# Kernel optimization log

Measured on AMD Instinct MI355X. Metric: run time of the kernel, lower is better.

The kernel has to match this reference:

```python
import jax, jax.numpy as jnp
import numpy as np

N = 50000
E = 800000
IN_C, HID, HEADS, CLS = 128, 64, 5, 40
NEG_SLOPE = 0.2


def gat_conv(h, src, dst, W, a_src, a_dst, bias, heads, out_c, concat):
    n = h.shape[0]
    hp = (h @ W).reshape(n, heads, out_c)            # [N,H,C]
    a_s = jnp.sum(hp * a_src, axis=-1)               # [N,H]
    a_d = jnp.sum(hp * a_dst, axis=-1)               # [N,H]
    e = jax.nn.leaky_relu(a_s[src] + a_d[dst], NEG_SLOPE)  # [Etot,H]
    m = jax.ops.segment_max(e, dst, num_segments=n)  # segment softmax over dst
    e = jnp.exp(e - m[dst])
    s = jax.ops.segment_sum(e, dst, num_segments=n)
    alpha = e / (s[dst] + 1e-16)                     # [Etot,H]
    msg = hp[src] * alpha[:, :, None]                # [Etot,H,C]
    out = jax.ops.segment_sum(msg, dst, num_segments=n)
    if concat:
        out = out.reshape(n, heads * out_c)
    else:
        out = out.mean(axis=1)
    return out + bias


def setup_inputs() -> dict:
    key = jax.random.key(0)
    ks = jax.random.split(key, 12)
    x = jax.random.normal(ks[0], (N, IN_C), dtype=jnp.float32)
    edge_index = jax.random.randint(ks[1], (2, E), 0, N, dtype=jnp.int64)
    g = 0.1
    return {
        "x": x,
        "edge_index": edge_index,
        "emb_W": jax.random.normal(ks[2], (IN_C, HID), jnp.float32) * g,
        "emb_b": jnp.zeros((HID,), jnp.float32),
        "W1": jax.random.normal(ks[3], (HID, HEADS * HID), jnp.float32) * g,
        "att_src1": jax.random.normal(ks[4], (HEADS, HID), jnp.float32) * g,
        "att_dst1": jax.random.normal(ks[5], (HEADS, HID), jnp.float32) * g,
        "b1": jnp.zeros((HEADS * HID,), jnp.float32),
        "W2": jax.random.normal(ks[6], (HEADS * HID, HEADS * CLS), jnp.float32) * g,
        "att_src2": jax.random.normal(ks[7], (HEADS, CLS), jnp.float32) * g,
        "att_dst2": jax.random.normal(ks[8], (HEADS, CLS), jnp.float32) * g,
        "b2": jnp.zeros((CLS,), jnp.float32),
    }


def reference(x, edge_index, emb_W, emb_b, W1, att_src1, att_dst1, b1,
              W2, att_src2, att_dst2, b2):
    n = x.shape[0]
    loops = jnp.arange(n, dtype=edge_index.dtype)
    src = jnp.concatenate([edge_index[0], loops])  # PyG adds self-loops
    dst = jnp.concatenate([edge_index[1], loops])
    h = x @ emb_W + emb_b
    emb = h
    # dropout skipped (eval mode)
    h = jax.nn.elu(gat_conv(h, src, dst, W1, att_src1, att_dst1, b1, HEADS, HID, True))
    h = gat_conv(h, src, dst, W2, att_src2, att_dst2, b2, HEADS, CLS, False)
    return emb, jax.nn.log_softmax(h, axis=1)
```

## Files before the change

kernel.cpp:

```cpp
#include <hip/hip_runtime.h>
#include <math.h>

constexpr int N_NODES = 50000;
constexpr int E_EDGES = 800000;
constexpr int ETOT    = E_EDGES + N_NODES;
constexpr int IN_C    = 128;
constexpr int HID     = 64;
constexpr int HEADS   = 5;
constexpr int CLS     = 40;
constexpr int SLOTW   = 96;
constexpr float NEG_SLOPE = 0.2f;

typedef __attribute__((ext_vector_type(8))) short short8;
typedef __attribute__((ext_vector_type(4))) float float4v;
typedef __attribute__((ext_vector_type(2))) float f32x2;

__device__ __forceinline__ float lrelu(float v) {
    return v > 0.f ? v : NEG_SLOPE * v;
}
__device__ __forceinline__ float bf2f(unsigned short u) {
    return __uint_as_float(((unsigned)u) << 16);
}
__device__ __forceinline__ f32x2 bfp2f(unsigned u) {
    f32x2 r;
    r.x = __uint_as_float(u << 16);
    r.y = __uint_as_float(u & 0xFFFF0000u);
    return r;
}
__device__ __forceinline__ unsigned short f2bf(float f) {
    unsigned u = __float_as_uint(f);
    return (unsigned short)((u + 0x7fffu + ((u >> 16) & 1u)) >> 16);
}

__device__ __forceinline__ void pack_one(const float* __restrict__ B,
                                         unsigned short* __restrict__ Bp,
                                         int N, int KS, int t)
{
    int lane = t & 63;
    int f = (t >> 6) & 3;
    int rest = t >> 8;
    int ks = rest % KS;
    int nt = rest / KS;
    int n = nt * 64 + f * 16 + (lane & 15);
    int kbase = ks * 32 + (lane >> 4) * 8;
    unsigned short vals[8];
    #pragma unroll
    for (int j = 0; j < 8; j++) {
        float v = (n < N) ? B[(long)(kbase + j) * N + n] : 0.f;
        vals[j] = f2bf(v);
    }
    *(ushort4*)(Bp + (long)t * 8)     = make_ushort4(vals[0], vals[1], vals[2], vals[3]);
    *(ushort4*)(Bp + (long)t * 8 + 4) = make_ushort4(vals[4], vals[5], vals[6], vals[7]);
}

__global__ void build_graph(const int* __restrict__ ei, int* __restrict__ cnt,
                            unsigned short* __restrict__ slots,
                            const float* __restrict__ W0, const float* __restrict__ W1,
                            const float* __restrict__ W2,
                            const float* __restrict__ att1s, const float* __restrict__ att1d,
                            const float* __restrict__ att2s, const float* __restrict__ att2d,
                            unsigned short* __restrict__ Bp0,
                            unsigned short* __restrict__ Bp1,
                            unsigned short* __restrict__ Bp2,
                            float* __restrict__ u1s, float* __restrict__ u1d,
                            float* __restrict__ u2s, float* __restrict__ u2d)
{
    int t = blockIdx.x * blockDim.x + threadIdx.x;
    if (t < 13824) {
        if (t < 1024)      pack_one(W0, Bp0, 64,  4,  t);
        else if (t < 3584) pack_one(W1, Bp1, 320, 2,  t - 1024);
        else               pack_one(W2, Bp2, 200, 10, t - 3584);
    } else if (t < 14464) {
        int i = t - 13824;
        bool isd = i >= 320;
        int j = isd ? i - 320 : i;
        int h = j >> 6, k = j & 63;
        const float* att = isd ? att1d : att1s;
        float sum = 0.f;
        for (int c = 0; c < 64; c++)
            sum += W1[k * 320 + h * 64 + c] * att[h * 64 + c];
        (isd ? u1d : u1s)[j] = sum;
    } else if (t < 17664) {
        int i = t - 14464;
        bool isd = i >= 1600;
        int j = isd ? i - 1600 : i;
        int h = j / 320, k = j % 320;
        const float* att = isd ? att2d : att2s;
        float sum = 0.f;
        for (int c = 0; c < 40; c++)
            sum += W2[k * 200 + h * 40 + c] * att[h * 40 + c];
        (isd ? u2d : u2s)[j] = sum;
    }
    if (t >= ETOT) return;
    int s, d;
    if (t < E_EDGES) { s = ei[t]; d = ei[E_EDGES + t]; }
    else             { s = d = t - E_EDGES; }
    int pos = atomicAdd(&cnt[d], 1);
    if (pos < SLOTW) slots[d * SLOTW + pos] = (unsigned short)s;
}

__global__ __launch_bounds__(256) void gemm_mfma_emb(
    const float* __restrict__ A, const unsigned short* __restrict__ Bp,
    const float* __restrict__ bias,
    const float* __restrict__ u1s, const float* __restrict__ u1d,
    float* __restrict__ Cf, unsigned short* __restrict__ Cb,
    float* __restrict__ asd, int M)
{
    const int K = 128, KS = 4;
    const int w = threadIdx.x >> 6, lane = threadIdx.x & 63;
    const int cl = lane & 15, kq = lane >> 4;
    int rowA = blockIdx.x * 64 + w * 16 + cl;
    if (rowA >= M) rowA = M - 1;
    const float* ap = A + (long)rowA * K + kq * 8;
    const unsigned short* bp = Bp + lane * 8;
    float4v acc[4] = {};
    #pragma unroll
    for (int ks = 0; ks < KS; ks++) {
        float4 u0 = *(const float4*)(ap + ks * 32);
        float4 u1 = *(const float4*)(ap + ks * 32 + 4);
        short8 a;
        a[0] = f2bf(u0.x); a[1] = f2bf(u0.y); a[2] = f2bf(u0.z); a[3] = f2bf(u0.w);
        a[4] = f2bf(u1.x); a[5] = f2bf(u1.y); a[6] = f2bf(u1.z); a[7] = f2bf(u1.w);
        #pragma unroll
        for (int f = 0; f < 4; f++) {
            short8 b = *(const short8*)(bp + ks * 2048 + f * 512);
            acc[f] = __builtin_amdgcn_mfma_f32_16x16x32_bf16(a, b, acc[f], 0, 0, 0);
        }
    }
    int rbase = blockIdx.x * 64 + w * 16 + kq * 4;
    float bc4[4];
    #pragma unroll
    for (int f = 0; f < 4; f++) {
        int col = f * 16 + cl;
        float bc = bias[col];
        bc4[f] = bc;
        #pragma unroll
        for (int r = 0; r < 4; r++) {
            int row = rbase + r;
            if (row < M) {
                float v = acc[f][r] + bc;
                Cf[(long)row * 64 + col] = v;
                Cb[(long)row * 64 + col] = f2bf(v);
            }
        }
    }
    #pragma unroll
    for (int h = 0; h < HEADS; h++) {
        float us[4], ud[4];
        #pragma unroll
        for (int f = 0; f < 4; f++) {
            us[f] = u1s[h * 64 + f * 16 + cl];
            ud[f] = u1d[h * 64 + f * 16 + cl];
        }
        #pragma unroll
        for (int r = 0; r < 4; r++) {
            float ps = 0.f, pd = 0.f;
            #pragma unroll
            for (int f = 0; f < 4; f++) {
                float v = acc[f][r] + bc4[f];
                ps += v * us[f];
                pd += v * ud[f];
            }
            #pragma unroll
            for (int off = 1; off < 16; off <<= 1) {
                ps += __shfl_xor(ps, off);
                pd += __shfl_xor(pd, off);
            }
            int row = rbase + r;
            if (cl == 0 && row < M) {
                asd[row * 16 + h]     = ps;
                asd[row * 16 + 8 + h] = pd;
            }
        }
    }
}

__global__ __launch_bounds__(256) void aggr1_new(
    const int* __restrict__ cnt, const unsigned short* __restrict__ slots,
    const float* __restrict__ asd,
    const unsigned short* __restrict__ emb, unsigned short* __restrict__ e_out)
{
    __shared__ float alph[4][64 * 8];
    int wid = (blockIdx.x * blockDim.x + threadIdx.x) >> 6;
    int w = threadIdx.x >> 6;
    int lane = threadIdx.x & 63;
    if (wid >= N_NODES) return;
    int deg = cnt[wid];
    if (deg > SLOTW) deg = SLOTW;
    const unsigned short* myslot = slots + wid * SLOTW;

    float adh[HEADS];
    #pragma unroll
    for (int h = 0; h < HEADS; h++) adh[h] = asd[wid * 16 + 8 + h];

    const char* embB = (const char*)emb;

    if (deg <= 64) {
        bool has = lane < deg;
        int s = has ? (int)myslot[lane] : 0;
        int rowoff = s * 128;
        float4 s4 = *(const float4*)(asd + s * 16);
        float  s5 = asd[s * 16 + 4];
        float v[HEADS], mx[HEADS], sm[HEADS];
        v[0] = has ? lrelu(s4.x + adh[0]) : -1e30f;
        v[1] = has ? lrelu(s4.y + adh[1]) : -1e30f;
        v[2] = has ? lrelu(s4.z + adh[2]) : -1e30f;
        v[3] = has ? lrelu(s4.w + adh[3]) : -1e30f;
        v[4] = has ? lrelu(s5   + adh[4]) : -1e30f;
        #pragma unroll
        for (int h = 0; h < HEADS; h++) mx[h] = v[h];
        if (deg <= 32) {
            #pragma unroll
            for (int h = 0; h < HEADS; h++)
                #pragma unroll
                for (int off = 16; off; off >>= 1)
                    mx[h] = fmaxf(mx[h], __shfl_xor(mx[h], off));
        } else {
            #pragma unroll
            for (int h = 0; h < HEADS; h++)
                #pragma unroll
                for (int off = 32; off; off >>= 1)
                    mx[h] = fmaxf(mx[h], __shfl_xor(mx[h], off));
        }
        #pragma unroll
        for (int h = 0; h < HEADS; h++) {
            float e = has ? __expf(v[h] - mx[h]) : 0.f;
            v[h] = e;
            sm[h] = e;
        }
        if (deg <= 32) {
            #pragma unroll
            for (int h = 0; h < HEADS; h++)
                #pragma unroll
                for (int off = 16; off; off >>= 1)
                    sm[h] += __shfl_xor(sm[h], off);
        } else {
            #pragma unroll
            for (int h = 0; h < HEADS; h++)
                #pragma unroll
                for (int off = 32; off; off >>= 1)
                    sm[h] += __shfl_xor(sm[h], off);
        }
        #pragma unroll
        for (int h = 0; h < HEADS; h++)
            alph[w][lane * 8 + h] = v[h] / (sm[h] + 1e-16f);

        const int g = lane >> 4, cl16 = lane & 15;
        f32x2 av[HEADS][2] = {};
        int nE8 = (deg + 7) & ~7;
        for (int i = 0; i < nE8; i += 8) {
            int e0 = i + g, e1 = i + 4 + g;
            int off0 = __shfl(rowoff, e0);
            int off1 = __shfl(rowoff, e1);
            uint2 q0 = *(const uint2*)(embB + off0 + cl16 * 8);
            uint2 q1 = *(const uint2*)(embB + off1 + cl16 * 8);
            float4 b0 = *(const float4*)&alph[w][e0 * 8];
            float  b4 = alph[w][e0 * 8 + 4];
            float4 c0 = *(const float4*)&alph[w][e1 * 8];
            float  c4 = alph[w][e1 * 8 + 4];
            f32x2 f0a = bfp2f(q0.x), f0b = bfp2f(q0.y);
            f32x2 f1a = bfp2f(q1.x), f1b = bfp2f(q1.y);
            av[0][0] += f0a * b0.x; av[0][1] += f0b * b0.x;
            av[1][0] += f0a * b0.y; av[1][1] += f0b * b0.y;
            av[2][0] += f0a * b0.z; av[2][1] += f0b * b0.z;
            av[3][0] += f0a * b0.w; av[3][1] += f0b * b0.w;
            av[4][0] += f0a * b4;   av[4][1] += f0b * b4;
            av[0][0] += f1a * c0.x; av[0][1] += f1b * c0.x;
            av[1][0] += f1a * c0.y; av[1][1] += f1b * c0.y;
            av[2][0] += f1a * c0.z; av[2][1] += f1b * c0.z;
            av[3][0] += f1a * c0.w; av[3][1] += f1b * c0.w;
            av[4][0] += f1a * c4;   av[4][1] += f1b * c4;
        }
        #pragma unroll
        for (int h = 0; h < HEADS; h++)
            #pragma unroll
            for (int p = 0; p < 2; p++) {
                float tx = av[h][p].x, ty = av[h][p].y;
                tx += __shfl_xor(tx, 16); tx += __shfl_xor(tx, 32);
                ty += __shfl_xor(ty, 16); ty += __shfl_xor(ty, 32);
                av[h][p].x = tx; av[h][p].y = ty;
            }
        if (g == 0) {
            #pragma unroll
            for (int h = 0; h < HEADS; h++) {
                ushort4 o = make_ushort4(f2bf(av[h][0].x), f2bf(av[h][0].y),
                                         f2bf(av[h][1].x), f2bf(av[h][1].y));
                *(ushort4*)(e_out + (long)wid * 320 + h * 64 + cl16 * 4) = o;
            }
        }
    } else {
        float acc[HEADS] = {};
        float mx[HEADS], inv[HEADS], sm[HEADS] = {};
        #pragma unroll
        for (int h = 0; h < HEADS; h++) mx[h] = -1e30f;
        for (int e = lane; e < deg; e += 64) {
            int s = myslot[e];
            #pragma unroll
            for (int h = 0; h < HEADS; h++)
                mx[h] = fmaxf(mx[h], lrelu(asd[s * 16 + h] + adh[h]));
        }
        #pragma unroll
        for (int h = 0; h < HEADS; h++)
            #pragma unroll
            for (int off = 32; off; off >>= 1)
                mx[h] = fmaxf(mx[h], __shfl_xor(mx[h], off));
        for (int e = lane; e < deg; e += 64) {
            int s = myslot[e];
            #pragma unroll
            for (int h = 0; h < HEADS; h++)
                sm[h] += __expf(lrelu(asd[s * 16 + h] + adh[h]) - mx[h]);
        }
        #pragma unroll
        for (int h = 0; h < HEADS; h++) {
            #pragma unroll
            for (int off = 32; off; off >>= 1)
                sm[h] += __shfl_xor(sm[h], off);
            inv[h] = 1.f / (sm[h] + 1e-16f);
        }
        for (int e = 0; e < deg; e++) {
            int s0 = myslot[e];
            float fv = bf2f(*(const unsigned short*)(embB + s0 * 128 + lane * 2));
            #pragma unroll
            for (int h = 0; h < HEADS; h++) {
                float a0 = __expf(lrelu(asd[s0 * 16 + h] + adh[h]) - mx[h]) * inv[h];
                acc[h] += fv * a0;
            }
        }
        #pragma unroll
        for (int h = 0; h < HEADS; h++)
            e_out[(long)wid * 320 + h * 64 + lane] = f2bf(acc[h]);
    }
}

__global__ __launch_bounds__(256) void gemm_mix_l2(
    const unsigned short* __restrict__ A, const unsigned short* __restrict__ Bp1,
    const unsigned short* __restrict__ Bp2, const float* __restrict__ bias,
    const float* __restrict__ u2s, const float* __restrict__ u2d,
    unsigned short* __restrict__ hp2, float* __restrict__ asd, int M)
{
    constexpr int LDP = 328;
    __shared__ unsigned short tile[64 * LDP];
    const int w = threadIdx.x >> 6, lane = threadIdx.x & 63;
    const int cl = lane & 15, kq = lane >> 4;
    int rowA = blockIdx.x * 64 + w * 16 + cl;
    if (rowA >= M) rowA = M - 1;
    const unsigned short* ap = A + (long)rowA * 320;
    const unsigned short* bp1 = Bp1 + lane * 8;

    float4v acc[20] = {};
    #pragma unroll
    for (int nt = 0; nt < 5; nt++)
        #pragma unroll
        for (int ks = 0; ks < 2; ks++) {
            short8 a = *(const short8*)(ap + nt * 64 + ks * 32 + kq * 8);
            #pragma unroll
            for (int f = 0; f < 4; f++) {
                short8 b = *(const short8*)(bp1 + (nt * 2 + ks) * 2048 + f * 512);
                acc[nt * 4 + f] =
                    __builtin_amdgcn_mfma_f32_16x16x32_bf16(a, b, acc[nt * 4 + f], 0, 0, 0);
            }
        }
    int rbase = blockIdx.x * 64 + w * 16 + kq * 4;
    const int lrow = w * 16 + kq * 4;
    #pragma unroll
    for (int nt = 0; nt < 5; nt++)
        #pragma unroll
        for (int f = 0; f < 4; f++) {
            int col = nt * 64 + f * 16 + cl;
            float bc = bias[col];
            #pragma unroll
            for (int r = 0; r < 4; r++) {
                float v = acc[nt * 4 + f][r] + bc;
                v = v > 0.f ? v : __expf(v) - 1.f;
                acc[nt * 4 + f][r] = v;
                tile[(lrow + r) * LDP + col] = f2bf(v);
            }
        }
    #pragma unroll
    for (int h = 0; h < HEADS; h++) {
        float us[20], ud[20];
        #pragma unroll
        for (int nt = 0; nt < 5; nt++)
            #pragma unroll
            for (int f = 0; f < 4; f++) {
                us[nt * 4 + f] = u2s[h * 320 + nt * 64 + f * 16 + cl];
                ud[nt * 4 + f] = u2d[h * 320 + nt * 64 + f * 16 + cl];
            }
        #pragma unroll
        for (int r = 0; r < 4; r++) {
            float ps = 0.f, pd = 0.f;
            #pragma unroll
            for (int j = 0; j < 20; j++) {
                ps += acc[j][r] * us[j];
                pd += acc[j][r] * ud[j];
            }
            #pragma unroll
            for (int off = 1; off < 16; off <<= 1) {
                ps += __shfl_xor(ps, off);
                pd += __shfl_xor(pd, off);
            }
            int row = rbase + r;
            if (cl == 0 && row < M) {
                asd[row * 16 + h]     = ps;
                asd[row * 16 + 8 + h] = pd;
            }
        }
    }

    const unsigned short* bp2 = Bp2 + lane * 8;
    const unsigned short* arow = tile + (w * 16 + cl) * LDP;
    float4v acc2[16] = {};
    #pragma unroll
    for (int ks = 0; ks < 10; ks++) {
        short8 a2 = *(const short8*)(arow + ks * 32 + kq * 8);
        #pragma unroll
        for (int nt = 0; nt < 4; nt++)
            #pragma unroll
            for (int f = 0; f < 4; f++) {
                short8 b = *(const short8*)(bp2 + (nt * 10 + ks) * 2048 + f * 512);
                acc2[nt * 4 + f] =
                    __builtin_amdgcn_mfma_f32_16x16x32_bf16(a2, b, acc2[nt * 4 + f], 0, 0, 0);
            }
    }
    #pragma unroll
    for (int nt = 0; nt < 4; nt++)
        #pragma unroll
        for (int f = 0; f < 4; f++) {
            int col = nt * 64 + f * 16 + cl;
            if (col >= 200) continue;
            #pragma unroll
            for (int r = 0; r < 4; r++) {
                int row = rbase + r;
                if (row < M) hp2[(long)row * 200 + col] = f2bf(acc2[nt * 4 + f][r]);
            }
        }
}

__global__ __launch_bounds__(256) void aggr2_fused(
    const int* __restrict__ cnt, const unsigned short* __restrict__ slots,
    const float* __restrict__ asd,
    const unsigned short* __restrict__ hp, const float* __restrict__ bias,
    float* __restrict__ out)
{
    __shared__ float alph[4][320];
    int wid = (blockIdx.x * blockDim.x + threadIdx.x) >> 6;
    int w = threadIdx.x >> 6;
    int lane = threadIdx.x & 63;
    if (wid >= N_NODES) return;
    int deg = cnt[wid];
    if (deg > SLOTW) deg = SLOTW;
    const unsigned short* myslot = slots + wid * SLOTW;

    float adh[HEADS];
    #pragma unroll
    for (int h = 0; h < HEADS; h++) adh[h] = asd[wid * 16 + 8 + h];

    const bool act = lane < 50;
    const int ch4 = lane * 4;
    const int hq  = act ? lane / 10 : 0;
    const char* hpB = (const char*)hp;
    f32x2 acc01 = {0.f, 0.f}, acc23 = {0.f, 0.f};

    if (deg <= 64) {
        bool has = lane < deg;
        int s = has ? (int)myslot[lane] : 0;
        int rowoff = s * 400;
        float4 s4 = *(const float4*)(asd + s * 16);
        float  s5 = asd[s * 16 + 4];
        float v[HEADS], mx[HEADS], sm[HEADS];
        v[0] = has ? lrelu(s4.x + adh[0]) : -1e30f;
        v[1] = has ? lrelu(s4.y + adh[1]) : -1e30f;
        v[2] = has ? lrelu(s4.z + adh[2]) : -1e30f;
        v[3] = has ? lrelu(s4.w + adh[3]) : -1e30f;
        v[4] = has ? lrelu(s5   + adh[4]) : -1e30f;
        #pragma unroll
        for (int h = 0; h < HEADS; h++) mx[h] = v[h];
        if (deg <= 32) {
            #pragma unroll
            for (int h = 0; h < HEADS; h++)
                #pragma unroll
                for (int off = 16; off; off >>= 1)
                    mx[h] = fmaxf(mx[h], __shfl_xor(mx[h], off));
        } else {
            #pragma unroll
            for (int h = 0; h < HEADS; h++)
                #pragma unroll
                for (int off = 32; off; off >>= 1)
                    mx[h] = fmaxf(mx[h], __shfl_xor(mx[h], off));
        }
        #pragma unroll
        for (int h = 0; h < HEADS; h++) {
            float e = has ? __expf(v[h] - mx[h]) : 0.f;
            v[h] = e;
            sm[h] = e;
        }
        if (deg <= 32) {
            #pragma unroll
            for (int h = 0; h < HEADS; h++)
                #pragma unroll
                for (int off = 16; off; off >>= 1)
                    sm[h] += __shfl_xor(sm[h], off);
        } else {
            #pragma unroll
            for (int h = 0; h < HEADS; h++)
                #pragma unroll
                for (int off = 32; off; off >>= 1)
                    sm[h] += __shfl_xor(sm[h], off);
        }
        if (has) {
            #pragma unroll
            for (int h = 0; h < HEADS; h++)
                alph[w][lane * 5 + h] = 0.2f * v[h] / (sm[h] + 1e-16f);
        }
        int i = 0;
        for (; i + 7 < deg; i += 8) {
            uint2 q[8]; float a[8];
            #pragma unroll
            for (int k = 0; k < 8; k++) {
                int off = __shfl(rowoff, i + k);
                q[k] = act ? *(const uint2*)(hpB + off + ch4 * 2)
                           : make_uint2(0u, 0u);
                a[k] = alph[w][(i + k) * 5 + hq];
            }
            #pragma unroll
            for (int k = 0; k < 8; k++) {
                f32x2 fa = bfp2f(q[k].x), fb = bfp2f(q[k].y);
                acc01 += fa * a[k];
                acc23 += fb * a[k];
            }
        }
        for (; i < deg; i++) {
            int off = __shfl(rowoff, i);
            if (act) {
                uint2 q0 = *(const uint2*)(hpB + off + ch4 * 2);
                float a0 = alph[w][i * 5 + hq];
                f32x2 fa = bfp2f(q0.x), fb = bfp2f(q0.y);
                acc01 += fa * a0;
                acc23 += fb * a0;
            }
        }
    } else {
        float mx[HEADS], inv[HEADS], sm[HEADS] = {};
        #pragma unroll
        for (int h = 0; h < HEADS; h++) mx[h] = -1e30f;
        for (int e = lane; e < deg; e += 64) {
            int s = myslot[e];
            #pragma unroll
            for (int h = 0; h < HEADS; h++)
                mx[h] = fmaxf(mx[h], lrelu(asd[s * 16 + h] + adh[h]));
        }
        #pragma unroll
        for (int h = 0; h < HEADS; h++)
            #pragma unroll
            for (int off = 32; off; off >>= 1)
                mx[h] = fmaxf(mx[h], __shfl_xor(mx[h], off));
        for (int e = lane; e < deg; e += 64) {
            int s = myslot[e];
            #pragma unroll
            for (int h = 0; h < HEADS; h++)
                sm[h] += __expf(lrelu(asd[s * 16 + h] + adh[h]) - mx[h]);
        }
        #pragma unroll
        for (int h = 0; h < HEADS; h++) {
            #pragma unroll
            for (int off = 32; off; off >>= 1)
                sm[h] += __shfl_xor(sm[h], off);
            inv[h] = 0.2f / (sm[h] + 1e-16f);
        }
        for (int e = 0; e < deg; e++) {
            int s0 = myslot[e];
            if (act) {
                uint2 q0 = *(const uint2*)(hpB + s0 * 400 + ch4 * 2);
                float a0 = __expf(lrelu(asd[s0 * 16 + hq] + adh[hq]) - mx[hq]) * inv[hq];
                f32x2 fa = bfp2f(q0.x), fb = bfp2f(q0.y);
                acc01 += fa * a0;
                acc23 += fb * a0;
            }
        }
    }

    float acc0 = acc01.x, acc1 = acc01.y, acc2 = acc23.x, acc3 = acc23.y;
    float r0 = acc0, r1 = acc1, r2 = acc2, r3 = acc3;
    #pragma unroll
    for (int h5 = 1; h5 < 5; h5++) {
        int sl = (lane + 10 * h5) & 63;
        r0 += __shfl(acc0, sl);
        r1 += __shfl(acc1, sl);
        r2 += __shfl(acc2, sl);
        r3 += __shfl(acc3, sl);
    }

    float vb0 = -1e30f, vb1 = -1e30f, vb2 = -1e30f, vb3 = -1e30f;
    if (lane < 10) {
        vb0 = r0 + bias[ch4 + 0];
        vb1 = r1 + bias[ch4 + 1];
        vb2 = r2 + bias[ch4 + 2];
        vb3 = r3 + bias[ch4 + 3];
    }
    float mxv = fmaxf(fmaxf(vb0, vb1), fmaxf(vb2, vb3));
    #pragma unroll
    for (int off = 32; off; off >>= 1)
        mxv = fmaxf(mxv, __shfl_xor(mxv, off));
    float sme = 0.f;
    if (lane < 10)
        sme = __expf(vb0 - mxv) + __expf(vb1 - mxv) +
              __expf(vb2 - mxv) + __expf(vb3 - mxv);
    #pragma unroll
    for (int off = 32; off; off >>= 1)
        sme += __shfl_xor(sme, off);
    float ls = mxv + __logf(sme);
    if (lane < 10) {
        float4 o = make_float4(vb0 - ls, vb1 - ls, vb2 - ls, vb3 - ls);
        *(float4*)(out + (long)wid * CLS + ch4) = o;
    }
}

extern "C" void kernel_launch(void* const* d_in, const int* in_sizes, int n_in,
                              void* d_out, int out_size, void* d_ws, size_t ws_size,
                              hipStream_t stream)
{
    const float* x     = (const float*)d_in[0];
    const int*   ei    = (const int*)d_in[1];
    const float* emb_W = (const float*)d_in[2];
    const float* emb_b = (const float*)d_in[3];
    const float* W1    = (const float*)d_in[4];
    const float* as1   = (const float*)d_in[5];
    const float* ad1   = (const float*)d_in[6];
    const float* b1    = (const float*)d_in[7];
    const float* W2    = (const float*)d_in[8];
    const float* as2   = (const float*)d_in[9];
    const float* ad2   = (const float*)d_in[10];
    const float* b2    = (const float*)d_in[11];

    float* out_emb = (float*)d_out;
    float* out_cls = (float*)d_out + (size_t)N_NODES * HID;

    char* ws = (char*)d_ws;
    unsigned short* e_agg  = (unsigned short*)(ws);
    unsigned short* hp2b   = (unsigned short*)(ws + 32000000);
    float*          asd1   = (float*)(ws + 52000000);
    float*          asd2   = (float*)(ws + 55200000);
    unsigned short* embb   = (unsigned short*)(ws + 64000000);
    unsigned short* Bp0    = (unsigned short*)(ws + 74400000);
    unsigned short* Bp1    = (unsigned short*)(ws + 74500000);
    unsigned short* Bp2    = (unsigned short*)(ws + 74600000);
    float*          u1s    = (float*)(ws + 74800000);
    float*          u1d    = (float*)(ws + 74810000);
    float*          u2s    = (float*)(ws + 74820000);
    float*          u2d    = (float*)(ws + 74830000);
    int*            cnt    = (int*)(ws + 74840000);
    unsigned short* slots  = (unsigned short*)(ws + 75100000);

    const dim3 blk(256);
    const int eb  = (ETOT + 255) / 256;
    const int nb4 = (N_NODES + 3) / 4;
    const int mgrid = (N_NODES + 63) / 64;

    hipMemsetAsync(cnt, 0, (size_t)N_NODES * 4, stream);
    build_graph<<<eb, blk, 0, stream>>>(ei, cnt, slots, emb_W, W1, W2,
                                        as1, ad1, as2, ad2,
                                        Bp0, Bp1, Bp2, u1s, u1d, u2s, u2d);

    gemm_mfma_emb<<<mgrid, blk, 0, stream>>>(x, Bp0, emb_b, u1s, u1d,
                                             out_emb, embb, asd1, N_NODES);

    aggr1_new<<<nb4, blk, 0, stream>>>(cnt, slots, asd1, embb, e_agg);

    gemm_mix_l2<<<mgrid, blk, 0, stream>>>(e_agg, Bp1, Bp2, b1, u2s, u2d,
                                           hp2b, asd2, N_NODES);

    aggr2_fused<<<nb4, blk, 0, stream>>>(cnt, slots, asd2, hp2b, b2, out_cls);
}
```

Baseline: 364.7 us.

## Split layer-2 GEMM across wave pairs and compute attention logits via MFMA

Restructures the fused layer-1 transform + layer-2 GEMM kernel so each block handles 32 rows, with two waves per 16-row band splitting the N dimension of both GEMMs and sharing the ELU output through LDS with a block barrier. The per-head attention projections (previously scalar dot products plus shuffles over 20 accumulators) are folded into an extra packed bf16 B matrix, so they come out of one additional MFMA column tile. This cuts per-wave register pressure (launch bounds raised to 5 waves) and scalar work. In exchange it adds a __syncthreads and computes the attention logits in bf16 precision rather than fp32.

```diff
diff --git a/kernel.cpp b/kernel.cpp
--- a/kernel.cpp
+++ b/kernel.cpp
@@ -63,7 +63,7 @@
                             unsigned short* __restrict__ Bp1,
                             unsigned short* __restrict__ Bp2,
                             float* __restrict__ u1s, float* __restrict__ u1d,
-                            float* __restrict__ u2s, float* __restrict__ u2d)
+                            unsigned short* __restrict__ Bs)
 {
     int t = blockIdx.x * blockDim.x + threadIdx.x;
     if (t < 13824) {
@@ -80,16 +80,27 @@
         for (int c = 0; c < 64; c++)
             sum += W1[k * 320 + h * 64 + c] * att[h * 64 + c];
         (isd ? u1d : u1s)[j] = sum;
-    } else if (t < 17664) {
+    } else if (t < 15104) {
         int i = t - 14464;
-        bool isd = i >= 1600;
-        int j = isd ? i - 1600 : i;
-        int h = j / 320, k = j % 320;
-        const float* att = isd ? att2d : att2s;
-        float sum = 0.f;
-        for (int c = 0; c < 40; c++)
-            sum += W2[k * 200 + h * 40 + c] * att[h * 40 + c];
-        (isd ? u2d : u2s)[j] = sum;
+        int lane = i & 63, ks = i >> 6;
+        int n = lane & 15, kq = lane >> 4;
+        unsigned short vals[8];
+        #pragma unroll
+        for (int j = 0; j < 8; j++) {
+            int k = ks * 32 + kq * 8 + j;
+            float sum = 0.f;
+            if (n < 5) {
+                for (int c = 0; c < 40; c++)
+                    sum += W2[k * 200 + n * 40 + c] * att2s[n * 40 + c];
+            } else if (n >= 8 && n < 13) {
+                int h = n - 8;
+                for (int c = 0; c < 40; c++)
+                    sum += W2[k * 200 + h * 40 + c] * att2d[h * 40 + c];
+            }
+            vals[j] = f2bf(sum);
+        }
+        *(ushort4*)(Bs + (long)i * 8)     = make_ushort4(vals[0], vals[1], vals[2], vals[3]);
+        *(ushort4*)(Bs + (long)i * 8 + 4) = make_ushort4(vals[4], vals[5], vals[6], vals[7]);
     }
     if (t >= ETOT) return;
     int s, d;
@@ -332,106 +343,120 @@
     }
 }
 
-__global__ __launch_bounds__(256) void gemm_mix_l2(
+__global__ __launch_bounds__(256, 5) void gemm_mix_l2(
     const unsigned short* __restrict__ A, const unsigned short* __restrict__ Bp1,
     const unsigned short* __restrict__ Bp2, const float* __restrict__ bias,
-    const float* __restrict__ u2s, const float* __restrict__ u2d,
+    const unsigned short* __restrict__ Bs,
     unsigned short* __restrict__ hp2, float* __restrict__ asd, int M)
 {
     constexpr int LDP = 328;
-    __shared__ unsigned short tile[64 * LDP];
-    const int w = threadIdx.x >> 6, lane = threadIdx.x & 63;
+    __shared__ unsigned short tile[32 * LDP];
+    const int wid = threadIdx.x >> 6, lane = threadIdx.x & 63;
+    const int band = wid >> 1, half = wid & 1;
     const int cl = lane & 15, kq = lane >> 4;
-    int rowA = blockIdx.x * 64 + w * 16 + cl;
+    int rowA = blockIdx.x * 32 + band * 16 + cl;
     if (rowA >= M) rowA = M - 1;
     const unsigned short* ap = A + (long)rowA * 320;
     const unsigned short* bp1 = Bp1 + lane * 8;
 
-    float4v acc[20] = {};
-    #pragma unroll
-    for (int nt = 0; nt < 5; nt++)
-        #pragma unroll
-        for (int ks = 0; ks < 2; ks++) {
-            short8 a = *(const short8*)(ap + nt * 64 + ks * 32 + kq * 8);
+    const int rbase = blockIdx.x * 32 + band * 16 + kq * 4;
+    const int lrow = band * 16 + kq * 4;
+
+    if (half == 0) {
+        float4v acc[12] = {};
+        #pragma unroll
+        for (int i = 0; i < 3; i++)
+            #pragma unroll
+            for (int ks = 0; ks < 2; ks++) {
+                short8 a = *(const short8*)(ap + i * 64 + ks * 32 + kq * 8);
+                #pragma unroll
+                for (int f = 0; f < 4; f++) {
+                    short8 b = *(const short8*)(bp1 + (i * 2 + ks) * 2048 + f * 512);
+                    acc[i * 4 + f] =
+                        __builtin_amdgcn_mfma_f32_16x16x32_bf16(a, b, acc[i * 4 + f], 0, 0, 0);
+                }
+            }
+        #pragma unroll
+        for (int i = 0; i < 3; i++)
             #pragma unroll
             for (int f = 0; f < 4; f++) {
-                short8 b = *(const short8*)(bp1 + (nt * 2 + ks) * 2048 + f * 512);
-                acc[nt * 4 + f] =
-                    __builtin_amdgcn_mfma_f32_16x16x32_bf16(a, b, acc[nt * 4 + f], 0, 0, 0);
-            }
-        }
-    int rbase = blockIdx.x * 64 + w * 16 + kq * 4;
-    const int lrow = w * 16 + kq * 4;
-    #pragma unroll
-    for (int nt = 0; nt < 5; nt++)
-        #pragma unroll
-        for (int f = 0; f < 4; f++) {
-            int col = nt * 64 + f * 16 + cl;
-            float bc = bias[col];
-            #pragma unroll
-            for (int r = 0; r < 4; r++) {
-                float v = acc[nt * 4 + f][r] + bc;
-                v = v > 0.f ? v : __expf(v) - 1.f;
-                acc[nt * 4 + f][r] = v;
-                tile[(lrow + r) * LDP + col] = f2bf(v);
-            }
-        }
-    #pragma unroll
-    for (int h = 0; h < HEADS; h++) {
-        float us[20], ud[20];
-        #pragma unroll
-        for (int nt = 0; nt < 5; nt++)
+                int col = i * 64 + f * 16 + cl;
+                float bc = bias[col];
+                #pragma unroll
+                for (int r = 0; r < 4; r++) {
+                    float v = acc[i * 4 + f][r] + bc;
+                    v = v > 0.f ? v : __expf(v) - 1.f;
+                    tile[(lrow + r) * LDP + col] = f2bf(v);
+                }
+            }
+    } else {
+        float4v acc[8] = {};
+        #pragma unroll
+        for (int i = 0; i < 2; i++)
+            #pragma unroll
+            for (int ks = 0; ks < 2; ks++) {
+                short8 a = *(const short8*)(ap + (3 + i) * 64 + ks * 32 + kq * 8);
+                #pragma unroll
+                for (int f = 0; f < 4; f++) {
+                    short8 b = *(const short8*)(bp1 + ((3 + i) * 2 + ks) * 2048 + f * 512);
+                    acc[i * 4 + f] =
+                        __builtin_amdgcn_mfma_f32_16x16x32_bf16(a, b, acc[i * 4 + f], 0, 0, 0);
+                }
+            }
+        #pragma unroll
+        for (int i = 0; i < 2; i++)
             #pragma unroll
             for (int f = 0; f < 4; f++) {
-                us[nt * 4 + f] = u2s[h * 320 + nt * 64 + f * 16 + cl];
-                ud[nt * 4 + f] = u2d[h * 320 + nt * 64 + f * 16 + cl];
-            }
-        #pragma unroll
-        for (int r = 0; r < 4; r++) {
-            float ps = 0.f, pd = 0.f;
-            #pragma unroll
-            for (int j = 0; j < 20; j++) {
-                ps += acc[j][r] * us[j];
-                pd += acc[j][r] * ud[j];
-            }
-            #pragma unroll
-            for (int off = 1; off < 16; off <<= 1) {
-                ps += __shfl_xor(ps, off);
-                pd += __shfl_xor(pd, off);
-            }
-            int row = rbase + r;
-            if (cl == 0 && row < M) {
-                asd[row * 16 + h]     = ps;
-                asd[row * 16 + 8 + h] = pd;
-            }
-        }
-    }
-
+                int col = (3 + i) * 64 + f * 16 + cl;
+                float bc = bias[col];
+                #pragma unroll
+                for (int r = 0; r < 4; r++) {
+                    float v = acc[i * 4 + f][r] + bc;
+                    v = v > 0.f ? v : __expf(v) - 1.f;
+                    tile[(lrow + r) * LDP + col] = f2bf(v);
+                }
+            }
+    }
+    __syncthreads();
+
+    const unsigned short* arow = tile + (band * 16 + cl) * LDP;
     const unsigned short* bp2 = Bp2 + lane * 8;
-    const unsigned short* arow = tile + (w * 16 + cl) * LDP;
-    float4v acc2[16] = {};
+    const unsigned short* bs  = Bs + lane * 8;
+    float4v acc2[8] = {};
+    float4v accs = {};
     #pragma unroll
     for (int ks = 0; ks < 10; ks++) {
         short8 a2 = *(const short8*)(arow + ks * 32 + kq * 8);
-        #pragma unroll
-        for (int nt = 0; nt < 4; nt++)
+        if (half == 0) {
+            short8 b = *(const short8*)(bs + ks * 512);
+            accs = __builtin_amdgcn_mfma_f32_16x16x32_bf16(a2, b, accs, 0, 0, 0);
+        }
+        #pragma unroll
+        for (int nt2 = 0; nt2 < 2; nt2++)
             #pragma unroll
             for (int f = 0; f < 4; f++) {
-                short8 b = *(const short8*)(bp2 + (nt * 10 + ks) * 2048 + f * 512);
-                acc2[nt * 4 + f] =
-                    __builtin_amdgcn_mfma_f32_16x16x32_bf16(a2, b, acc2[nt * 4 + f], 0, 0, 0);
-            }
-    }
-    #pragma unroll
-    for (int nt = 0; nt < 4; nt++)
+                short8 b = *(const short8*)(bp2 + (((half * 2 + nt2) * 10 + ks) * 2048) + f * 512);
+                acc2[nt2 * 4 + f] =
+                    __builtin_amdgcn_mfma_f32_16x16x32_bf16(a2, b, acc2[nt2 * 4 + f], 0, 0, 0);
+            }
+    }
+    if (half == 0) {
+        #pragma unroll
+        for (int r = 0; r < 4; r++) {
+            int row = rbase + r;
+            if (row < M) asd[row * 16 + cl] = accs[r];
+        }
+    }
+    #pragma unroll
+    for (int nt2 = 0; nt2 < 2; nt2++)
         #pragma unroll
         for (int f = 0; f < 4; f++) {
-            int col = nt * 64 + f * 16 + cl;
+            int col = (half * 2 + nt2) * 64 + f * 16 + cl;
             if (col >= 200) continue;
             #pragma unroll
             for (int r = 0; r < 4; r++) {
                 int row = rbase + r;
-                if (row < M) hp2[(long)row * 200 + col] = f2bf(acc2[nt * 4 + f][r]);
+                if (row < M) hp2[(long)row * 200 + col] = f2bf(acc2[nt2 * 4 + f][r]);
             }
         }
 }
@@ -646,28 +671,28 @@
     unsigned short* Bp2    = (unsigned short*)(ws + 74600000);
     float*          u1s    = (float*)(ws + 74800000);
     float*          u1d    = (float*)(ws + 74810000);
-    float*          u2s    = (float*)(ws + 74820000);
-    float*          u2d    = (float*)(ws + 74830000);
+    unsigned short* Bs     = (unsigned short*)(ws + 74820000);
     int*            cnt    = (int*)(ws + 74840000);
     unsigned short* slots  = (unsigned short*)(ws + 75100000);
 
     const dim3 blk(256);
-    const int eb  = (ETOT + 255) / 256;
-    const int nb4 = (N_NODES + 3) / 4;
-    const int mgrid = (N_NODES + 63) / 64;
+    const int eb   = (ETOT + 255) / 256;
+    const int nb4  = (N_NODES + 3) / 4;
+    const int mgrid  = (N_NODES + 63) / 64;
+    const int mgrid2 = (N_NODES + 31) / 32;
 
     hipMemsetAsync(cnt, 0, (size_t)N_NODES * 4, stream);
     build_graph<<<eb, blk, 0, stream>>>(ei, cnt, slots, emb_W, W1, W2,
                                         as1, ad1, as2, ad2,
-                                        Bp0, Bp1, Bp2, u1s, u1d, u2s, u2d);
+                                        Bp0, Bp1, Bp2, u1s, u1d, Bs);
 
     gemm_mfma_emb<<<mgrid, blk, 0, stream>>>(x, Bp0, emb_b, u1s, u1d,
                                              out_emb, embb, asd1, N_NODES);
 
     aggr1_new<<<nb4, blk, 0, stream>>>(cnt, slots, asd1, embb, e_agg);
 
-    gemm_mix_l2<<<mgrid, blk, 0, stream>>>(e_agg, Bp1, Bp2, b1, u2s, u2d,
-                                           hp2b, asd2, N_NODES);
+    gemm_mix_l2<<<mgrid2, blk, 0, stream>>>(e_agg, Bp1, Bp2, b1, Bs,
+                                            hp2b, asd2, N_NODES);
 
     aggr2_fused<<<nb4, blk, 0, stream>>>(cnt, slots, asd2, hp2b, b2, out_cls);
 }
```

Result: faster. 343.0 us (-5.9%).
